# Performance work log

Measured on AMD Instinct MI355X. Metric: run time of the kernel, lower is better.

Reference implementation:

```python
import jax, jax.numpy as jnp
import numpy as np

SIZES = [4096, 4096, 4096, 4096]  # input, hidden0, hidden1, output


def setup_inputs() -> dict:
    key = jax.random.key(0)
    ks = jax.random.split(key, 16)
    inp = {"x": jax.random.normal(ks[0], (SIZES[0],), dtype=jnp.float32)}
    ki = 1
    for i in range(3):
        fan_in, fan_out = SIZES[i], SIZES[i + 1]
        bound = 1.0 / np.sqrt(fan_in)
        inp[f"W{i}"] = jax.random.uniform(ks[ki], (fan_out, fan_in), minval=-bound, maxval=bound, dtype=jnp.float32)
        inp[f"b{i}"] = jax.random.uniform(ks[ki + 1], (fan_out,), minval=-bound, maxval=bound, dtype=jnp.float32)
        # hebbian_coeff initialized to ones in __init__, but allow generic values
        inp[f"H{i}"] = jax.random.normal(ks[ki + 2], (fan_out, fan_in, 5), dtype=jnp.float32) * 0.01
        ki += 3
    return inp


def _forward(x, Ws, bs, Hs):
    # MLP forward collecting per-layer activations (states)
    states = [x]
    h = x
    for W, b in zip(Ws[:-1], bs[:-1]):
        h = jnp.tanh(h @ W.T + b)
        states.append(h)
    y = h @ Ws[-1].T + bs[-1]
    states.append(jax.nn.sigmoid(y))  # env_name == 'CartPole-v1'
    # Hebbian ABCD update. NOTE: in the original, delta_weights aliases
    # layer.weight, so every element is overwritten with delta and the
    # subsequent `+=` produces new_weight = 2 * delta (old weight discarded).
    new_Ws = []
    for W, H, pre, post in zip(Ws, Hs, states[:-1], states[1:]):
        A, B, C, D, E = (H[..., m] for m in range(5))  # each [out, in]
        pre_b = pre[None, :]    # [1, in]
        post_b = post[:, None]  # [out, 1]
        delta = A * (B * pre_b * post_b + C * pre_b + D * post_b + E)
        new_Ws.append(2.0 * delta)
    return (y, *new_Ws)


def reference(x, W0, b0, W1, b1, W2, b2, H0, H1, H2):
    return _forward(x, [W0, W1, W2], [b0, b1, b2], [H0, H1, H2])
```

## Files before the change

### kernel.cpp

```cpp
#include <hip/hip_runtime.h>
#include <math.h>

#define N 4096

typedef float f32x4 __attribute__((ext_vector_type(4)));

__global__ __launch_bounds__(256) void mv_kernel(const float* __restrict__ W,
                                                 const float* __restrict__ b,
                                                 const float* __restrict__ x,
                                                 float* __restrict__ out,
                                                 float* __restrict__ y_out,
                                                 int mode) {
    const int p   = blockIdx.x;
    const int tid = threadIdx.x;
    __shared__ float red[4];

    const f32x4* xv = reinterpret_cast<const f32x4*>(x);
    const f32x4* Wr = reinterpret_cast<const f32x4*>(W + (size_t)p * N);

    float acc = 0.0f;
#pragma unroll
    for (int i = 0; i < 4; ++i) {
        const int j = tid + i * 256;
        f32x4 w4 = Wr[j];
        f32x4 x4 = xv[j];
        acc += w4.x * x4.x + w4.y * x4.y + w4.z * x4.z + w4.w * x4.w;
    }
#pragma unroll
    for (int off = 32; off > 0; off >>= 1)
        acc += __shfl_down(acc, off, 64);
    if ((tid & 63) == 0) red[tid >> 6] = acc;
    __syncthreads();
    if (tid == 0) {
        const float v = red[0] + red[1] + red[2] + red[3] + b[p];
        if (mode == 0) {
            out[p] = tanhf(v);
        } else {
            y_out[p] = v;
            out[p]   = 1.0f / (1.0f + expf(-v));
        }
    }
}

__global__ __launch_bounds__(256) void hebb_all(const float* __restrict__ H0,
                                                const float* __restrict__ H1,
                                                const float* __restrict__ H2,
                                                const float* __restrict__ pre0,
                                                const float* __restrict__ pre1,
                                                const float* __restrict__ pre2,
                                                const float* __restrict__ post0,
                                                const float* __restrict__ post1,
                                                const float* __restrict__ post2,
                                                float* __restrict__ o0,
                                                float* __restrict__ o1,
                                                float* __restrict__ o2) {
    const int L    = blockIdx.x >> 14;
    const int bidx = blockIdx.x & 16383;

    const float* H;  const float* pre;  const float* post;  float* outW;
    if (L == 0)      { H = H0; pre = pre0; post = post0; outW = o0; }
    else if (L == 1) { H = H1; pre = pre1; post = post1; outW = o1; }
    else             { H = H2; pre = pre2; post = post2; outW = o2; }

    const int idx = bidx * 256 + threadIdx.x;
    const int p   = idx >> 10;
    const int q0  = (idx & 1023) << 2;

    const size_t base = ((size_t)p * N + q0) * 5;
    const f32x4* h4   = reinterpret_cast<const f32x4*>(H + base);
    f32x4 v0 = h4[0];
    f32x4 v1 = h4[1];
    f32x4 v2 = h4[2];
    f32x4 v3 = h4[3];
    f32x4 v4 = h4[4];

    const float po = post[p];
    const f32x4 pr = *reinterpret_cast<const f32x4*>(pre + q0);

    f32x4 o;
    o.x = 2.0f * v0.x * (v0.y * pr.x * po + v0.z * pr.x + v0.w * po + v1.x);
    o.y = 2.0f * v1.y * (v1.z * pr.y * po + v1.w * pr.y + v2.x * po + v2.y);
    o.z = 2.0f * v2.z * (v2.w * pr.z * po + v3.x * pr.z + v3.y * po + v3.z);
    o.w = 2.0f * v3.w * (v4.x * pr.w * po + v4.y * pr.w + v4.z * po + v4.w);

    *reinterpret_cast<f32x4*>(outW + (size_t)p * N + q0) = o;
}

extern "C" void kernel_launch(void* const* d_in, const int* in_sizes, int n_in,
                              void* d_out, int out_size, void* d_ws, size_t ws_size,
                              hipStream_t stream) {
    const float* x  = (const float*)d_in[0];
    const float* W0 = (const float*)d_in[1];
    const float* b0 = (const float*)d_in[2];
    const float* H0 = (const float*)d_in[3];
    const float* W1 = (const float*)d_in[4];
    const float* b1 = (const float*)d_in[5];
    const float* H1 = (const float*)d_in[6];
    const float* W2 = (const float*)d_in[7];
    const float* b2 = (const float*)d_in[8];
    const float* H2 = (const float*)d_in[9];

    float* out = (float*)d_out;
    float* y   = out;
    float* oW0 = out + N;
    float* oW1 = oW0 + (size_t)N * N;
    float* oW2 = oW1 + (size_t)N * N;

    float* s  = (float*)d_ws;
    float* s1 = s;
    float* s2 = s + N;
    float* s3 = s + 2 * N;

    const dim3 mvGrid(N), mvBlock(256);

    hipLaunchKernelGGL(mv_kernel, mvGrid, mvBlock, 0, stream, W0, b0, x,  s1, (float*)nullptr, 0);
    hipLaunchKernelGGL(mv_kernel, mvGrid, mvBlock, 0, stream, W1, b1, s1, s2, (float*)nullptr, 0);
    hipLaunchKernelGGL(mv_kernel, mvGrid, mvBlock, 0, stream, W2, b2, s2, s3, y, 1);

    const dim3 hGrid(3 * 16384), hBlock(256);
    hipLaunchKernelGGL(hebb_all, hGrid, hBlock, 0, stream,
                       H0, H1, H2, x, s1, s2, s1, s2, s3, oW0, oW1, oW2);
}
```

Baseline: 255.4 us.

## Overlap Hebbian updates with later matvec layers in fused launches

Reorders the schedule so the Hebbian update for layer i runs in the same launch as the matvec for layer i+1, since its inputs are already available. The first blocks of each fused launch compute two matvec rows each, and the remaining blocks process Hebbian elements. Only the last layer's Hebbian update runs on its own. The aim is to hide the small latency-bound matvec launches under the bandwidth-bound Hebbian traffic, at the cost of some branch divergence across blocks and uneven block durations.

```diff
diff --git a/kernel.cpp b/kernel.cpp
--- a/kernel.cpp
+++ b/kernel.cpp
@@ -5,16 +5,13 @@
 
 typedef float f32x4 __attribute__((ext_vector_type(4)));
 
-__global__ __launch_bounds__(256) void mv_kernel(const float* __restrict__ W,
-                                                 const float* __restrict__ b,
-                                                 const float* __restrict__ x,
-                                                 float* __restrict__ out,
-                                                 float* __restrict__ y_out,
-                                                 int mode) {
-    const int p   = blockIdx.x;
+__device__ __forceinline__ void mv_row(const float* __restrict__ W,
+                                       const float* __restrict__ b,
+                                       const float* __restrict__ x,
+                                       float* __restrict__ out,
+                                       float* __restrict__ y_out,
+                                       int p, int mode, float* red) {
     const int tid = threadIdx.x;
-    __shared__ float red[4];
-
     const f32x4* xv = reinterpret_cast<const f32x4*>(x);
     const f32x4* Wr = reinterpret_cast<const f32x4*>(W + (size_t)p * N);
 
@@ -40,31 +37,15 @@
             out[p]   = 1.0f / (1.0f + expf(-v));
         }
     }
+    __syncthreads();
 }
 
-__global__ __launch_bounds__(256) void hebb_all(const float* __restrict__ H0,
-                                                const float* __restrict__ H1,
-                                                const float* __restrict__ H2,
-                                                const float* __restrict__ pre0,
-                                                const float* __restrict__ pre1,
-                                                const float* __restrict__ pre2,
-                                                const float* __restrict__ post0,
-                                                const float* __restrict__ post1,
-                                                const float* __restrict__ post2,
-                                                float* __restrict__ o0,
-                                                float* __restrict__ o1,
-                                                float* __restrict__ o2) {
-    const int L    = blockIdx.x >> 14;
-    const int bidx = blockIdx.x & 16383;
-
-    const float* H;  const float* pre;  const float* post;  float* outW;
-    if (L == 0)      { H = H0; pre = pre0; post = post0; outW = o0; }
-    else if (L == 1) { H = H1; pre = pre1; post = post1; outW = o1; }
-    else             { H = H2; pre = pre2; post = post2; outW = o2; }
-
-    const int idx = bidx * 256 + threadIdx.x;
-    const int p   = idx >> 10;
-    const int q0  = (idx & 1023) << 2;
+__device__ __forceinline__ void hebb_group(const float* __restrict__ H,
+                                           const float* __restrict__ pre,
+                                           const float* __restrict__ post,
+                                           float* __restrict__ outW, int idx) {
+    const int p  = idx >> 10;
+    const int q0 = (idx & 1023) << 2;
 
     const size_t base = ((size_t)p * N + q0) * 5;
     const f32x4* h4   = reinterpret_cast<const f32x4*>(H + base);
@@ -84,6 +65,44 @@
     o.w = 2.0f * v3.w * (v4.x * pr.w * po + v4.y * pr.w + v4.z * po + v4.w);
 
     *reinterpret_cast<f32x4*>(outW + (size_t)p * N + q0) = o;
+}
+
+__global__ __launch_bounds__(256) void mv_kernel(const float* __restrict__ W,
+                                                 const float* __restrict__ b,
+                                                 const float* __restrict__ x,
+                                                 float* __restrict__ out,
+                                                 float* __restrict__ y_out,
+                                                 int mode) {
+    __shared__ float red[4];
+    mv_row(W, b, x, out, y_out, blockIdx.x, mode, red);
+}
+
+__global__ __launch_bounds__(256) void mv_hebb(const float* __restrict__ W,
+                                               const float* __restrict__ b,
+                                               const float* __restrict__ xin,
+                                               float* __restrict__ mv_out,
+                                               float* __restrict__ y_out,
+                                               int mode,
+                                               const float* __restrict__ H,
+                                               const float* __restrict__ pre,
+                                               const float* __restrict__ post,
+                                               float* __restrict__ outW) {
+    __shared__ float red[4];
+    if (blockIdx.x < 2048) {
+        mv_row(W, b, xin, mv_out, y_out, blockIdx.x * 2,     mode, red);
+        mv_row(W, b, xin, mv_out, y_out, blockIdx.x * 2 + 1, mode, red);
+    } else {
+        const int idx = (blockIdx.x - 2048) * 256 + threadIdx.x;
+        hebb_group(H, pre, post, outW, idx);
+    }
+}
+
+__global__ __launch_bounds__(256) void hebb_kernel(const float* __restrict__ H,
+                                                   const float* __restrict__ pre,
+                                                   const float* __restrict__ post,
+                                                   float* __restrict__ outW) {
+    const int idx = blockIdx.x * 256 + threadIdx.x;
+    hebb_group(H, pre, post, outW, idx);
 }
 
 extern "C" void kernel_launch(void* const* d_in, const int* in_sizes, int n_in,
@@ -111,13 +130,17 @@
     float* s2 = s + N;
     float* s3 = s + 2 * N;
 
-    const dim3 mvGrid(N), mvBlock(256);
+    hipLaunchKernelGGL(mv_kernel, dim3(N), dim3(256), 0, stream,
+                       W0, b0, x, s1, (float*)nullptr, 0);
 
-    hipLaunchKernelGGL(mv_kernel, mvGrid, mvBlock, 0, stream, W0, b0, x,  s1, (float*)nullptr, 0);
-    hipLaunchKernelGGL(mv_kernel, mvGrid, mvBlock, 0, stream, W1, b1, s1, s2, (float*)nullptr, 0);
-    hipLaunchKernelGGL(mv_kernel, mvGrid, mvBlock, 0, stream, W2, b2, s2, s3, y, 1);
+    hipLaunchKernelGGL(mv_hebb, dim3(18432), dim3(256), 0, stream,
+                       W1, b1, s1, s2, (float*)nullptr, 0,
+                       H0, x, s1, oW0);
 
-    const dim3 hGrid(3 * 16384), hBlock(256);
-    hipLaunchKernelGGL(hebb_all, hGrid, hBlock, 0, stream,
-                       H0, H1, H2, x, s1, s2, s1, s2, s3, oW0, oW1, oW2);
+    hipLaunchKernelGGL(mv_hebb, dim3(18432), dim3(256), 0, stream,
+                       W2, b2, s2, s3, y, 1,
+                       H1, s1, s2, oW1);
+
+    hipLaunchKernelGGL(hebb_kernel, dim3(16384), dim3(256), 0, stream,
+                       H2, s2, s3, oW2);
 }
```

New measurement: 255.1 us. No clear change (-0.1%).
